# Performance work log

Measured on AMD Instinct MI355X. Metric: run time of the kernel, lower is better.

## Reference

```python
import jax, jax.numpy as jnp
import numpy as np
from jax import lax

EPS = 1e-5


def _conv(x, w, b, stride, pad):
    # x: [B,C,H,W], w: [O,I,kh,kw] (NCHW / OIHW, same as torch Conv2d)
    y = lax.conv_general_dilated(
        x, w, window_strides=stride,
        padding=[(pad[0], pad[0]), (pad[1], pad[1])],
        dimension_numbers=('NCHW', 'OIHW', 'NCHW'))
    return y + b[None, :, None, None]


def _bn(x, gamma, beta, mean, var):
    # BatchNorm2d in eval mode (running statistics)
    inv = gamma / jnp.sqrt(var + EPS)
    return x * inv[None, :, None, None] + (beta - mean * inv)[None, :, None, None]


def _mask_time(x, lens):
    # Vectorized replacement of the per-sample narrow/fill loop:
    # zero every time step >= lens[b] along the last axis.
    t = jnp.arange(x.shape[3])
    keep = (t[None, :] < lens[:, None]).astype(x.dtype)  # [B, W]
    return x * keep[:, None, None, :]


def _new_len(lens, kernel_w, stride_w, pad_w):
    # matches get_new_sequence_lengths for Conv2d with dilation 1
    return (lens + 2 * pad_w - (kernel_w - 1) - 1) // stride_w + 1


def _forward(inputs, seq_lengths,
             w1, b1, g1, be1, m1, v1,
             w2, b2, g2, be2, m2, v2):
    lens = seq_lengths.astype(jnp.int32)
    # layer 1: Conv2d(1,32,(41,11),(2,2),(20,5))
    x = _conv(inputs, w1, b1, (2, 2), (20, 5))
    lens = _new_len(lens, 11, 2, 5)
    x = _mask_time(x, lens)
    # BatchNorm2d(32) -> mask
    x = _mask_time(_bn(x, g1, be1, m1, v1), lens)
    # Hardtanh(0,20) -> mask
    x = _mask_time(jnp.clip(x, 0.0, 20.0), lens)
    # layer 2: Conv2d(32,32,(21,11),(2,1),(10,5))
    x = _conv(x, w2, b2, (2, 1), (10, 5))
    lens = _new_len(lens, 11, 1, 5)
    x = _mask_time(x, lens)
    x = _mask_time(_bn(x, g2, be2, m2, v2), lens)
    x = _mask_time(jnp.clip(x, 0.0, 20.0), lens)
    return x, lens


def setup_inputs() -> dict:
    key = jax.random.key(0)
    ks = jax.random.split(key, 8)
    inputs = jax.random.normal(ks[0], (32, 1, 161, 1024), dtype=jnp.float32)
    seq_lengths = jax.random.randint(ks[1], (32,), 1, 1024, dtype=jnp.int32)
    w1 = jax.random.normal(ks[2], (32, 1, 41, 11), dtype=jnp.float32) * 0.05
    b1 = jax.random.normal(ks[3], (32,), dtype=jnp.float32) * 0.05
    w2 = jax.random.normal(ks[4], (32, 32, 21, 11), dtype=jnp.float32) * 0.02
    b2 = jax.random.normal(ks[5], (32,), dtype=jnp.float32) * 0.05
    g1 = jnp.ones((32,), jnp.float32)
    be1 = jnp.zeros((32,), jnp.float32)
    m1 = jax.random.normal(ks[6], (32,), dtype=jnp.float32) * 0.1
    v1 = jnp.ones((32,), jnp.float32)
    g2 = jnp.ones((32,), jnp.float32)
    be2 = jnp.zeros((32,), jnp.float32)
    m2 = jax.random.normal(ks[7], (32,), dtype=jnp.float32) * 0.1
    v2 = jnp.ones((32,), jnp.float32)
    return {"inputs": inputs, "seq_lengths": seq_lengths,
            "w1": w1, "b1": b1, "g1": g1, "be1": be1, "m1": m1, "v1": v1,
            "w2": w2, "b2": b2, "g2": g2, "be2": be2, "m2": m2, "v2": v2}


def reference(inputs, seq_lengths, w1, b1, g1, be1, m1, v1,
              w2, b2, g2, be2, m2, v2):
    return _forward(inputs, seq_lengths, w1, b1, g1, be1, m1, v1,
                    w2, b2, g2, be2, m2, v2)
```

## Files before the change

kernel.cpp:

```cpp
#include <hip/hip_runtime.h>
#include <math.h>

#define B_    32
#define H_IN  161
#define W_IN  1024
#define C1_   32
#define H1_   81
#define W1_   512
#define C2_   32
#define H2_   41
#define W2_   512

#define OUT_X_SZ ((size_t)B_ * C2_ * H2_ * W2_)

#define WF2_B    0u
#define WF1_B    563200u
#define SCSH_B   609280u
#define LENS1_B  609792u
#define XG_B     609920u

#define WF2_N    281600
#define WF1_N    23040

typedef __bf16 v8bf __attribute__((ext_vector_type(8)));
typedef float v16f __attribute__((ext_vector_type(16)));

static __device__ __forceinline__ unsigned short f2bf(float f) {
    unsigned int u = __float_as_uint(f);
    unsigned int r = (u + 0x7fffu + ((u >> 16) & 1u)) >> 16;
    return (unsigned short)r;
}

__global__ void prep_kernel(const float* __restrict__ w1, const float* __restrict__ b1,
                            const float* __restrict__ g1, const float* __restrict__ be1,
                            const float* __restrict__ m1, const float* __restrict__ v1,
                            const float* __restrict__ w2, const float* __restrict__ b2,
                            const float* __restrict__ g2, const float* __restrict__ be2,
                            const float* __restrict__ m2, const float* __restrict__ v2,
                            const int* __restrict__ lens,
                            unsigned short* __restrict__ wf1, unsigned short* __restrict__ wf2,
                            float* __restrict__ scsh, int* __restrict__ lens1,
                            float* __restrict__ out_lens)
{
    const int i = blockIdx.x * blockDim.x + threadIdx.x;
    const int stride = gridDim.x * blockDim.x;

    for (int idx = i; idx < WF2_N; idx += stride) {
        int j  = idx & 7;
        int l  = (idx >> 3) & 63;
        int f  = idx >> 9;
        int ch = f & 1;
        int kwkh = f >> 1;
        int kw  = kwkh % 11;
        int khp = kwkh / 11;
        int kh  = khp - 2;
        int oc = l & 31;
        int c  = ch * 16 + ((l >> 5) << 3) + j;
        wf2[idx] = (kh >= 0 && kh < 21)
                 ? f2bf(w2[((oc * 32 + c) * 21 + kh) * 11 + kw]) : (unsigned short)0;
    }
    for (int idx = i; idx < WF1_N; idx += stride) {
        int j   = idx & 7;
        int l   = (idx >> 3) & 63;
        int khp = idx >> 9;
        int kh  = khp - 2;
        int k   = ((l >> 5) << 3) + j;
        int oc  = l & 31;
        wf1[idx] = (k < 11 && kh >= 0 && kh < 41)
                 ? f2bf(w1[oc * 451 + kh * 11 + k]) : (unsigned short)0;
    }
    if (i < 32) {
        float s1 = g1[i] / sqrtf(v1[i] + 1e-5f);
        scsh[i]      = s1;
        scsh[32 + i] = b1[i] * s1 + be1[i] - m1[i] * s1;
        float s2 = g2[i] / sqrtf(v2[i] + 1e-5f);
        scsh[64 + i] = s2;
        scsh[96 + i] = b2[i] * s2 + be2[i] - m2[i] * s2;
        int l1 = (lens[i] - 1) / 2 + 1;
        if (l1 > W1_) l1 = W1_;
        lens1[i] = l1;
        out_lens[i] = (float)l1;
    }
}

#define S1ROWS 55
#define S1U    264

__global__ __launch_bounds__(256, 2) void conv1_mfma(
    const float* __restrict__ x,
    const unsigned short* __restrict__ wf1,
    const float* __restrict__ scsh,
    const int* __restrict__ lens1,
    unsigned short* __restrict__ xg)
{
    const int t    = threadIdx.x;
    const int lane = t & 63;
    const int l31  = lane & 31;
    const int lhi  = lane >> 5;
    const int wv   = t >> 6;
    const int w0   = blockIdx.x * 256;
    const int seg  = blockIdx.y;
    const int b    = blockIdx.z;

    __shared__ unsigned int slab[S1ROWS * S1U];

    const int rbase = 16 * seg - 20;
    const int cb    = 2 * w0 - 5;
    const float* xb = x + (size_t)b * (H_IN * W_IN);

    for (int rho = wv; rho < S1ROWS; rho += 4) {
        const int r = rbase + rho;
        const bool rowok = (r >= 0) && (r < H_IN);
        const float* src = xb + (size_t)r * W_IN;
        unsigned int* drow = &slab[rho * S1U];
#pragma unroll
        for (int j = 0; j < 4; ++j) {
            const int cp = lane + 64 * j;
            const int c  = cb + 2 * cp;
            float a0 = 0.f, a1 = 0.f;
            if (rowok) {
                if ((unsigned)c < (unsigned)W_IN)       a0 = src[c];
                if ((unsigned)(c + 1) < (unsigned)W_IN) a1 = src[c + 1];
            }
            drow[cp] = (unsigned int)f2bf(a0) | ((unsigned int)f2bf(a1) << 16);
        }
        if (lane < 8) {
            const int cp = lane + 256;
            const int c  = cb + 2 * cp;
            float a0 = 0.f, a1 = 0.f;
            if (rowok) {
                if ((unsigned)c < (unsigned)W_IN)       a0 = src[c];
                if ((unsigned)(c + 1) < (unsigned)W_IN) a1 = src[c + 1];
            }
            drow[cp] = (unsigned int)f2bf(a0) | ((unsigned int)f2bf(a1) << 16);
        }
    }
    __syncthreads();

    const uint4* wf1q = (const uint4*)wf1;
    const int dwbase  = wv * 64 + l31 + 4 * lhi;
    const int l1      = lens1[b];

    for (int q = 0; q < 4; ++q) {
        const int pr = seg * 4 + q;
        if (pr > 40) break;
        const int h0 = pr * 2;
        const bool h1ok = (h0 + 1) < H1_;

        v16f acc[2][2];
#pragma unroll
        for (int hh = 0; hh < 2; ++hh)
#pragma unroll
            for (int nt = 0; nt < 2; ++nt)
#pragma unroll
                for (int qq = 0; qq < 16; ++qq) acc[hh][nt][qq] = 0.f;

        const unsigned int* base = &slab[(4 * q) * S1U];

        for (int kp = 0; kp < 43; ++kp) {
            uint4 a0u = wf1q[(kp + 2) * 32 + lane];
            uint4 a1u = wf1q[kp * 32 + lane];
            const unsigned int* bp = base + kp * S1U;
            uint4 bu0, bu1;
            {
                int dw = dwbase;
                bu0.x = bp[dw]; bu0.y = bp[dw + 1]; bu0.z = bp[dw + 2]; bu0.w = bp[dw + 3];
                dw += 32;
                bu1.x = bp[dw]; bu1.y = bp[dw + 1]; bu1.z = bp[dw + 2]; bu1.w = bp[dw + 3];
            }
            v8bf A0 = __builtin_bit_cast(v8bf, a0u);
            v8bf A1 = __builtin_bit_cast(v8bf, a1u);
            v8bf B0 = __builtin_bit_cast(v8bf, bu0);
            v8bf B1 = __builtin_bit_cast(v8bf, bu1);
            acc[0][0] = __builtin_amdgcn_mfma_f32_32x32x16_bf16(A0, B0, acc[0][0], 0, 0, 0);
            acc[0][1] = __builtin_amdgcn_mfma_f32_32x32x16_bf16(A0, B1, acc[0][1], 0, 0, 0);
            acc[1][0] = __builtin_amdgcn_mfma_f32_32x32x16_bf16(A1, B0, acc[1][0], 0, 0, 0);
            acc[1][1] = __builtin_amdgcn_mfma_f32_32x32x16_bf16(A1, B1, acc[1][1], 0, 0, 0);
        }

#pragma unroll
        for (int hh = 0; hh < 2; ++hh) {
            if (hh == 1 && !h1ok) break;
            const int h = h0 + hh;
#pragma unroll
            for (int nt = 0; nt < 2; ++nt) {
                const int w = w0 + wv * 64 + nt * 32 + l31;
                const bool keep = (w < l1);
                unsigned short* dp = xg + (((size_t)b * H1_ + h) * W1_ + w) * 32;
#pragma unroll
                for (int rq = 0; rq < 4; ++rq) {
                    unsigned int wd[2];
#pragma unroll
                    for (int d = 0; d < 2; ++d) {
                        int rg = rq * 4 + d * 2;
                        int oc = 8 * rq + 4 * lhi + d * 2;
                        float av0 = acc[hh][nt][rg];
                        float av1 = acc[hh][nt][rg + 1];
                        float v0 = fminf(fmaxf(fmaf(av0, scsh[oc],     scsh[32 + oc]), 0.f), 20.f);
                        float v1 = fminf(fmaxf(fmaf(av1, scsh[oc + 1], scsh[33 + oc]), 0.f), 20.f);
                        if (!keep) { v0 = 0.f; v1 = 0.f; }
                        wd[d] = (unsigned int)f2bf(v0) | ((unsigned int)f2bf(v1) << 16);
                    }
                    uint2 u; u.x = wd[0]; u.y = wd[1];
                    *(uint2*)(dp + 8 * rq + 4 * lhi) = u;
                }
            }
        }
    }
}

#define ROWB 21280

__global__ __launch_bounds__(256, 3) void conv2_mfma(
    const unsigned short* __restrict__ xg,
    const unsigned short* __restrict__ wf2,
    const float* __restrict__ scsh,
    const int* __restrict__ lens1,
    float* __restrict__ out)
{
    const int t    = threadIdx.x;
    const int lane = t & 63;
    const int l31  = lane & 31;
    const int lhi  = lane >> 5;
    const int wv   = t >> 6;

    const int id   = blockIdx.x;
    const int sid  = (id & 7) * 168 + (id >> 3);
    const int wblk = sid & 1;
    const int bh   = sid >> 1;
    const int hp   = bh % 21;
    const int b    = bh / 21;
    const int h0   = hp * 2;
    const bool h1ok = (h0 + 1) < H2_;
    const int w0B  = wblk << 8;

    __shared__ __align__(16) char sbuf[2 * ROWB];

    v16f acc[2][2];
#pragma unroll
    for (int hh = 0; hh < 2; ++hh)
#pragma unroll
        for (int nt = 0; nt < 2; ++nt)
#pragma unroll
            for (int q = 0; q < 16; ++q) acc[hh][nt][q] = 0.f;

    const int st_lds = (t >> 2) * 80 + (t & 3) * 16;
    const int rd_lds = (wv * 64 + l31) * 80 + lhi * 16;

    const unsigned short* xb = xg + (size_t)b * (H1_ * W1_ * 32);
    const int r0 = 2 * h0 - 10;

    {
        int r = r0;
        if (r >= 0 && r < H1_) {
            const unsigned short* xrow = xb + (size_t)r * (W1_ * 32);
#pragma unroll
            for (int it = 0; it < 5; ++it) {
                int i = t + it * 256;
                int wp = (i >> 2) + w0B - 5;
                uint4 z; z.x = z.y = z.z = z.w = 0u;
                if (i < 1064 && wp >= 0 && wp < W1_)
                    z = *(const uint4*)(xrow + (size_t)wp * 32 + (i & 3) * 8);
                if (i < 1064)
                    *(uint4*)(sbuf + st_lds + it * 5120) = z;
            }
        }
    }
    __syncthreads();

    const uint4* wq = (const uint4*)wf2;

    for (int kp = 0; kp < 23; ++kp) {
        const int p = kp & 1;
        const int rn = r0 + kp + 1;
        const bool stage_next = (kp < 22) && (rn >= 0) && (rn < H1_);

        uint4 g0, g1, g2, g3, g4;
        g0.x=g0.y=g0.z=g0.w=0u; g1=g0; g2=g0; g3=g0; g4=g0;
        if (stage_next) {
            const unsigned short* xrow = xb + (size_t)rn * (W1_ * 32);
            const int wbase = (t >> 2) + w0B - 5;
            const int ck = (t & 3) * 8;
            if (wbase >= 0 && wbase < W1_)                 g0 = *(const uint4*)(xrow + (size_t)wbase * 32 + ck);
            if (wbase + 64 >= 0 && wbase + 64 < W1_)       g1 = *(const uint4*)(xrow + (size_t)(wbase + 64) * 32 + ck);
            if (wbase + 128 < W1_)                         g2 = *(const uint4*)(xrow + (size_t)(wbase + 128) * 32 + ck);
            if (wbase + 192 < W1_)                         g3 = *(const uint4*)(xrow + (size_t)(wbase + 192) * 32 + ck);
            if (t < 40 && wbase + 256 < W1_)               g4 = *(const uint4*)(xrow + (size_t)(wbase + 256) * 32 + ck);
        }

        const int r = r0 + kp;
        if (r >= 0 && r < H1_) {
            const int f0 = (kp + 2) * 22;
            const int f1 = kp * 22;
            const char* bbase = sbuf + p * ROWB + rd_lds;
            __builtin_amdgcn_s_setprio(1);
#pragma unroll
            for (int kw = 0; kw < 11; ++kw) {
#pragma unroll
                for (int ch = 0; ch < 2; ++ch) {
                    uint4 a0u = wq[(f0 + kw * 2 + ch) * 64 + lane];
                    uint4 a1u = wq[(f1 + kw * 2 + ch) * 64 + lane];
                    uint4 b0u = *(const uint4*)(bbase + kw * 80 + ch * 32);
                    uint4 b1u = *(const uint4*)(bbase + 2560 + kw * 80 + ch * 32);
                    v8bf A0 = __builtin_bit_cast(v8bf, a0u);
                    v8bf A1 = __builtin_bit_cast(v8bf, a1u);
                    v8bf B0 = __builtin_bit_cast(v8bf, b0u);
                    v8bf B1 = __builtin_bit_cast(v8bf, b1u);
                    acc[0][0] = __builtin_amdgcn_mfma_f32_32x32x16_bf16(A0, B0, acc[0][0], 0, 0, 0);
                    acc[0][1] = __builtin_amdgcn_mfma_f32_32x32x16_bf16(A0, B1, acc[0][1], 0, 0, 0);
                    acc[1][0] = __builtin_amdgcn_mfma_f32_32x32x16_bf16(A1, B0, acc[1][0], 0, 0, 0);
                    acc[1][1] = __builtin_amdgcn_mfma_f32_32x32x16_bf16(A1, B1, acc[1][1], 0, 0, 0);
                }
            }
            __builtin_amdgcn_s_setprio(0);
        }

        if (stage_next) {
            char* wb = sbuf + (p ^ 1) * ROWB + st_lds;
            *(uint4*)(wb)            = g0;
            *(uint4*)(wb + 5120)     = g1;
            *(uint4*)(wb + 2 * 5120) = g2;
            *(uint4*)(wb + 3 * 5120) = g3;
            if (t < 40) *(uint4*)(wb + 4 * 5120) = g4;
        }
        __syncthreads();
    }

    const int l2 = lens1[b];
#pragma unroll
    for (int hh = 0; hh < 2; ++hh) {
        if (hh == 1 && !h1ok) break;
        const int h = h0 + hh;
#pragma unroll
        for (int nt = 0; nt < 2; ++nt) {
            const int w = w0B + wv * 64 + nt * 32 + l31;
            const bool keep = (w < l2);
#pragma unroll
            for (int reg = 0; reg < 16; ++reg) {
                const int oc = (reg & 3) + 8 * (reg >> 2) + 4 * lhi;
                float v = fmaf(acc[hh][nt][reg], scsh[64 + oc], scsh[96 + oc]);
                v = fminf(fmaxf(v, 0.f), 20.f);
                out[(((size_t)b * C2_ + oc) * H2_ + h) * W2_ + w] = keep ? v : 0.f;
            }
        }
    }
}

extern "C" void kernel_launch(void* const* d_in, const int* in_sizes, int n_in,
                              void* d_out, int out_size, void* d_ws, size_t ws_size,
                              hipStream_t stream) {
    const float* inputs = (const float*)d_in[0];
    const int*   slen   = (const int*)d_in[1];
    const float* w1 = (const float*)d_in[2];
    const float* b1 = (const float*)d_in[3];
    const float* g1 = (const float*)d_in[4];
    const float* be1 = (const float*)d_in[5];
    const float* m1 = (const float*)d_in[6];
    const float* v1 = (const float*)d_in[7];
    const float* w2 = (const float*)d_in[8];
    const float* b2 = (const float*)d_in[9];
    const float* g2 = (const float*)d_in[10];
    const float* be2 = (const float*)d_in[11];
    const float* m2 = (const float*)d_in[12];
    const float* v2 = (const float*)d_in[13];

    char* ws = (char*)d_ws;
    unsigned short* wf2  = (unsigned short*)(ws + WF2_B);
    unsigned short* wf1  = (unsigned short*)(ws + WF1_B);
    float*          scsh = (float*)(ws + SCSH_B);
    int*            lens1 = (int*)(ws + LENS1_B);
    unsigned short* xg   = (unsigned short*)(ws + XG_B);

    float* out_x    = (float*)d_out;
    float* out_lens = out_x + OUT_X_SZ;

    hipLaunchKernelGGL(prep_kernel, dim3(256), dim3(256), 0, stream,
                       w1, b1, g1, be1, m1, v1, w2, b2, g2, be2, m2, v2,
                       slen, wf1, wf2, scsh, lens1, out_lens);

    hipLaunchKernelGGL(conv1_mfma, dim3(2, 11, B_), dim3(256), 0, stream,
                       inputs, wf1, scsh, lens1, xg);

    hipLaunchKernelGGL(conv2_mfma, dim3(1344), dim3(256), 0, stream,
                       xg, wf2, scsh, lens1, out_x);
}
```

Before: 544.1 us.

## Restructure conv1 to one row-pair per block with double-buffered row streaming

Conv1 now computes a single output row-pair per block instead of four, streaming the 43 input rows through a small double-buffered LDS tile. The next rows are prefetched into registers while MFMAs run, and padding rows outside the input are skipped. This shrinks LDS use and raises block count and occupancy to hide load latency. In exchange, input rows are re-read by more blocks and there are more barriers per block.

```diff
diff --git a/kernel.cpp b/kernel.cpp
--- a/kernel.cpp
+++ b/kernel.cpp
@@ -83,10 +83,7 @@
     }
 }
 
-#define S1ROWS 55
-#define S1U    264
-
-__global__ __launch_bounds__(256, 2) void conv1_mfma(
+__global__ __launch_bounds__(256) void conv1_mfma(
     const float* __restrict__ x,
     const unsigned short* __restrict__ wf1,
     const float* __restrict__ scsh,
@@ -99,36 +96,48 @@
     const int lhi  = lane >> 5;
     const int wv   = t >> 6;
     const int w0   = blockIdx.x * 256;
-    const int seg  = blockIdx.y;
+    const int hp   = blockIdx.y;
     const int b    = blockIdx.z;
-
-    __shared__ unsigned int slab[S1ROWS * S1U];
-
-    const int rbase = 16 * seg - 20;
-    const int cb    = 2 * w0 - 5;
+    const int h0   = hp * 2;
+    const bool h1ok = (h0 + 1) < H1_;
+
+    __shared__ unsigned int srow[2][4][264];
+
+    v16f acc[2][2];
+#pragma unroll
+    for (int hh = 0; hh < 2; ++hh)
+#pragma unroll
+        for (int nt = 0; nt < 2; ++nt)
+#pragma unroll
+            for (int q = 0; q < 16; ++q) acc[hh][nt][q] = 0.f;
+
+    const int r0 = 2 * h0 - 20;
+    const int cb = 2 * w0 - 5;
     const float* xb = x + (size_t)b * (H_IN * W_IN);
 
-    for (int rho = wv; rho < S1ROWS; rho += 4) {
-        const int r = rbase + rho;
-        const bool rowok = (r >= 0) && (r < H_IN);
+    const int dwbase = wv * 64 + l31 + 4 * lhi;
+
+    {
+        const int r = r0 + wv;
+        const bool rok = (r >= 0) && (r < H_IN);
         const float* src = xb + (size_t)r * W_IN;
-        unsigned int* drow = &slab[rho * S1U];
-#pragma unroll
-        for (int j = 0; j < 4; ++j) {
-            const int cp = lane + 64 * j;
+        unsigned int* drow = &srow[0][wv][0];
+#pragma unroll
+        for (int jj = 0; jj < 4; ++jj) {
+            const int cp = lane + 64 * jj;
             const int c  = cb + 2 * cp;
             float a0 = 0.f, a1 = 0.f;
-            if (rowok) {
+            if (rok) {
                 if ((unsigned)c < (unsigned)W_IN)       a0 = src[c];
                 if ((unsigned)(c + 1) < (unsigned)W_IN) a1 = src[c + 1];
             }
             drow[cp] = (unsigned int)f2bf(a0) | ((unsigned int)f2bf(a1) << 16);
         }
         if (lane < 8) {
-            const int cp = lane + 256;
+            const int cp = 256 + lane;
             const int c  = cb + 2 * cp;
             float a0 = 0.f, a1 = 0.f;
-            if (rowok) {
+            if (rok) {
                 if ((unsigned)c < (unsigned)W_IN)       a0 = src[c];
                 if ((unsigned)(c + 1) < (unsigned)W_IN) a1 = src[c + 1];
             }
@@ -138,72 +147,97 @@
     __syncthreads();
 
     const uint4* wf1q = (const uint4*)wf1;
-    const int dwbase  = wv * 64 + l31 + 4 * lhi;
-    const int l1      = lens1[b];
-
-    for (int q = 0; q < 4; ++q) {
-        const int pr = seg * 4 + q;
-        if (pr > 40) break;
-        const int h0 = pr * 2;
-        const bool h1ok = (h0 + 1) < H1_;
-
-        v16f acc[2][2];
-#pragma unroll
-        for (int hh = 0; hh < 2; ++hh)
-#pragma unroll
-            for (int nt = 0; nt < 2; ++nt)
-#pragma unroll
-                for (int qq = 0; qq < 16; ++qq) acc[hh][nt][qq] = 0.f;
-
-        const unsigned int* base = &slab[(4 * q) * S1U];
-
-        for (int kp = 0; kp < 43; ++kp) {
-            uint4 a0u = wf1q[(kp + 2) * 32 + lane];
-            uint4 a1u = wf1q[kp * 32 + lane];
-            const unsigned int* bp = base + kp * S1U;
-            uint4 bu0, bu1;
-            {
-                int dw = dwbase;
-                bu0.x = bp[dw]; bu0.y = bp[dw + 1]; bu0.z = bp[dw + 2]; bu0.w = bp[dw + 3];
-                dw += 32;
-                bu1.x = bp[dw]; bu1.y = bp[dw + 1]; bu1.z = bp[dw + 2]; bu1.w = bp[dw + 3];
-            }
-            v8bf A0 = __builtin_bit_cast(v8bf, a0u);
-            v8bf A1 = __builtin_bit_cast(v8bf, a1u);
-            v8bf B0 = __builtin_bit_cast(v8bf, bu0);
-            v8bf B1 = __builtin_bit_cast(v8bf, bu1);
-            acc[0][0] = __builtin_amdgcn_mfma_f32_32x32x16_bf16(A0, B0, acc[0][0], 0, 0, 0);
-            acc[0][1] = __builtin_amdgcn_mfma_f32_32x32x16_bf16(A0, B1, acc[0][1], 0, 0, 0);
-            acc[1][0] = __builtin_amdgcn_mfma_f32_32x32x16_bf16(A1, B0, acc[1][0], 0, 0, 0);
-            acc[1][1] = __builtin_amdgcn_mfma_f32_32x32x16_bf16(A1, B1, acc[1][1], 0, 0, 0);
-        }
-
-#pragma unroll
-        for (int hh = 0; hh < 2; ++hh) {
-            if (hh == 1 && !h1ok) break;
-            const int h = h0 + hh;
-#pragma unroll
-            for (int nt = 0; nt < 2; ++nt) {
-                const int w = w0 + wv * 64 + nt * 32 + l31;
-                const bool keep = (w < l1);
-                unsigned short* dp = xg + (((size_t)b * H1_ + h) * W1_ + w) * 32;
-#pragma unroll
-                for (int rq = 0; rq < 4; ++rq) {
-                    unsigned int wd[2];
-#pragma unroll
-                    for (int d = 0; d < 2; ++d) {
-                        int rg = rq * 4 + d * 2;
-                        int oc = 8 * rq + 4 * lhi + d * 2;
-                        float av0 = acc[hh][nt][rg];
-                        float av1 = acc[hh][nt][rg + 1];
-                        float v0 = fminf(fmaxf(fmaf(av0, scsh[oc],     scsh[32 + oc]), 0.f), 20.f);
-                        float v1 = fminf(fmaxf(fmaf(av1, scsh[oc + 1], scsh[33 + oc]), 0.f), 20.f);
-                        if (!keep) { v0 = 0.f; v1 = 0.f; }
-                        wd[d] = (unsigned int)f2bf(v0) | ((unsigned int)f2bf(v1) << 16);
-                    }
-                    uint2 u; u.x = wd[0]; u.y = wd[1];
-                    *(uint2*)(dp + 8 * rq + 4 * lhi) = u;
+
+    for (int s = 0; s < 11; ++s) {
+        const int p = s & 1;
+
+        float sa[5][2];
+#pragma unroll
+        for (int jj = 0; jj < 5; ++jj) { sa[jj][0] = 0.f; sa[jj][1] = 0.f; }
+        const int kpn = 4 * (s + 1) + wv;
+        const int rn  = r0 + kpn;
+        const bool sv = (s < 10) && (kpn < 43) && (rn >= 0) && (rn < H_IN);
+        if (sv) {
+            const float* src = xb + (size_t)rn * W_IN;
+#pragma unroll
+            for (int jj = 0; jj < 4; ++jj) {
+                const int c = cb + 2 * (lane + 64 * jj);
+                if ((unsigned)c < (unsigned)W_IN)       sa[jj][0] = src[c];
+                if ((unsigned)(c + 1) < (unsigned)W_IN) sa[jj][1] = src[c + 1];
+            }
+            if (lane < 8) {
+                const int c = cb + 2 * (256 + lane);
+                if ((unsigned)c < (unsigned)W_IN)       sa[4][0] = src[c];
+                if ((unsigned)(c + 1) < (unsigned)W_IN) sa[4][1] = src[c + 1];
+            }
+        }
+
+#pragma unroll
+        for (int j = 0; j < 4; ++j) {
+            const int kp = 4 * s + j;
+            if (kp > 42) break;
+            const int r = r0 + kp;
+            if (r >= 0 && r < H_IN) {
+                uint4 a0u = wf1q[(kp + 2) * 32 + lane];
+                uint4 a1u = wf1q[kp * 32 + lane];
+                v8bf A0 = __builtin_bit_cast(v8bf, a0u);
+                v8bf A1 = __builtin_bit_cast(v8bf, a1u);
+                const unsigned int* bp = &srow[p][j][0];
+                uint4 bu0, bu1;
+                {
+                    int dw = dwbase;
+                    bu0.x = bp[dw]; bu0.y = bp[dw + 1]; bu0.z = bp[dw + 2]; bu0.w = bp[dw + 3];
+                    dw += 32;
+                    bu1.x = bp[dw]; bu1.y = bp[dw + 1]; bu1.z = bp[dw + 2]; bu1.w = bp[dw + 3];
                 }
+                v8bf B0 = __builtin_bit_cast(v8bf, bu0);
+                v8bf B1 = __builtin_bit_cast(v8bf, bu1);
+                acc[0][0] = __builtin_amdgcn_mfma_f32_32x32x16_bf16(A0, B0, acc[0][0], 0, 0, 0);
+                acc[0][1] = __builtin_amdgcn_mfma_f32_32x32x16_bf16(A0, B1, acc[0][1], 0, 0, 0);
+                acc[1][0] = __builtin_amdgcn_mfma_f32_32x32x16_bf16(A1, B0, acc[1][0], 0, 0, 0);
+                acc[1][1] = __builtin_amdgcn_mfma_f32_32x32x16_bf16(A1, B1, acc[1][1], 0, 0, 0);
+            }
+        }
+
+        if (sv) {
+            unsigned int* drow = &srow[p ^ 1][wv][0];
+#pragma unroll
+            for (int jj = 0; jj < 4; ++jj)
+                drow[lane + 64 * jj] =
+                    (unsigned int)f2bf(sa[jj][0]) | ((unsigned int)f2bf(sa[jj][1]) << 16);
+            if (lane < 8)
+                drow[256 + lane] =
+                    (unsigned int)f2bf(sa[4][0]) | ((unsigned int)f2bf(sa[4][1]) << 16);
+        }
+        __syncthreads();
+    }
+
+    const int l1 = lens1[b];
+#pragma unroll
+    for (int hh = 0; hh < 2; ++hh) {
+        if (hh == 1 && !h1ok) break;
+        const int h = h0 + hh;
+#pragma unroll
+        for (int nt = 0; nt < 2; ++nt) {
+            const int w = w0 + wv * 64 + nt * 32 + l31;
+            const bool keep = (w < l1);
+            unsigned short* dp = xg + (((size_t)b * H1_ + h) * W1_ + w) * 32;
+#pragma unroll
+            for (int rq = 0; rq < 4; ++rq) {
+                unsigned int wd[2];
+#pragma unroll
+                for (int d = 0; d < 2; ++d) {
+                    int rg = rq * 4 + d * 2;
+                    int oc = 8 * rq + 4 * lhi + d * 2;
+                    float av0 = acc[hh][nt][rg];
+                    float av1 = acc[hh][nt][rg + 1];
+                    float v0 = fminf(fmaxf(fmaf(av0, scsh[oc],     scsh[32 + oc]), 0.f), 20.f);
+                    float v1 = fminf(fmaxf(fmaf(av1, scsh[oc + 1], scsh[33 + oc]), 0.f), 20.f);
+                    if (!keep) { v0 = 0.f; v1 = 0.f; }
+                    wd[d] = (unsigned int)f2bf(v0) | ((unsigned int)f2bf(v1) << 16);
+                }
+                uint2 u; u.x = wd[0]; u.y = wd[1];
+                *(uint2*)(dp + 8 * rq + 4 * lhi) = u;
             }
         }
     }
@@ -378,7 +412,7 @@
                        w1, b1, g1, be1, m1, v1, w2, b2, g2, be2, m2, v2,
                        slen, wf1, wf2, scsh, lens1, out_lens);
 
-    hipLaunchKernelGGL(conv1_mfma, dim3(2, 11, B_), dim3(256), 0, stream,
+    hipLaunchKernelGGL(conv1_mfma, dim3(2, 41, B_), dim3(256), 0, stream,
                        inputs, wf1, scsh, lens1, xg);
 
     hipLaunchKernelGGL(conv2_mfma, dim3(1344), dim3(256), 0, stream,
```

Result: no change. 534.5 us (-1.8%).
